# Kernel tuning notes

Measured on AMD Instinct MI355X. Metric: run time of the kernel, lower is better.

Reference implementation:

```python
import jax, jax.numpy as jnp
import numpy as np

B, T, I, H, C = 8192, 28, 28, 128, 10


def setup_inputs() -> dict:
    key = jax.random.key(0)
    ks = jax.random.split(key, 7)
    s_ih = 1.0 / np.sqrt(H)
    return {
        "x": jax.random.normal(ks[0], (B, T, I), dtype=jnp.float32),
        "W_ih": jax.random.normal(ks[1], (4 * H, I), dtype=jnp.float32) * s_ih,
        "W_hh": jax.random.normal(ks[2], (4 * H, H), dtype=jnp.float32) * s_ih,
        "b_ih": jax.random.normal(ks[3], (4 * H,), dtype=jnp.float32) * s_ih,
        "b_hh": jax.random.normal(ks[4], (4 * H,), dtype=jnp.float32) * s_ih,
        "W_fc": jax.random.normal(ks[5], (C, H), dtype=jnp.float32) * s_ih,
        "b_fc": jnp.zeros((C,), dtype=jnp.float32),
    }


def reference(x, W_ih, W_hh, b_ih, b_hh, W_fc, b_fc):
    # x: [B, T, I]. PyTorch LSTM gate order: i, f, g, o.
    b = b_ih + b_hh  # [4H]
    # Precompute input projections for all timesteps: [T, B, 4H]
    x_proj = jnp.einsum("bti,gi->tbg", x, W_ih) + b
    h0 = jnp.zeros((x.shape[0], H), dtype=x.dtype)
    c0 = jnp.zeros_like(h0)

    def step(carry, xp_t):
        h, c = carry
        gates = xp_t + h @ W_hh.T  # [B, 4H]
        i_g, f_g, g_g, o_g = jnp.split(gates, 4, axis=-1)
        i_g = jax.nn.sigmoid(i_g)
        f_g = jax.nn.sigmoid(f_g)
        g_g = jnp.tanh(g_g)
        o_g = jax.nn.sigmoid(o_g)
        c = f_g * c + i_g * g_g
        h = o_g * jnp.tanh(c)
        return (h, c), None

    (h_last, _), _ = jax.lax.scan(step, (h0, c0), x_proj)
    # outputs[:, -1, :] == final hidden state; fc + relu
    return jax.nn.relu(h_last @ W_fc.T + b_fc)
```

## Files before the change

### kernel.cpp

```cpp
#include <hip/hip_runtime.h>
#include <math.h>

typedef __attribute__((ext_vector_type(8))) _Float16 half8;
typedef __attribute__((ext_vector_type(4))) _Float16 half4;
typedef __attribute__((ext_vector_type(4))) float    f32x4;

#define TSTEPS 28
#define IDIM   28
#define HDIM   128
#define NKC    5
#define TILE_B 16
#define CDIM   10

#if __has_builtin(__builtin_amdgcn_exp2f)
#define EXP2F(x) __builtin_amdgcn_exp2f(x)
#else
#define EXP2F(x) exp2f(x)
#endif
#if __has_builtin(__builtin_amdgcn_rcpf)
#define RCPF(x) __builtin_amdgcn_rcpf(x)
#else
#define RCPF(x) (1.0f / (x))
#endif

#define NLOG2E (-1.44269504f)
#define P2LOG2E (2.88539008f)

__global__ __launch_bounds__(256) void pack_w(const float* __restrict__ Wih,
                                              const float* __restrict__ Whh,
                                              const float* __restrict__ bih,
                                              const float* __restrict__ bhh,
                                              _Float16* __restrict__ P) {
    int e = blockIdx.x * 256 + threadIdx.x;
    if (e >= NKC * 4 * 8 * 64 * 8) return;
    int j  = e & 7;
    int ln = (e >> 3) & 63;
    int w  = (e >> 9) & 7;
    int t  = (e >> 12) & 3;
    int kc = e >> 14;
    int k  = kc * 32 + ((ln >> 4) << 3) + j;
    int u  = w * 16 + (ln & 15);
    int g  = t * HDIM + u;
    float v = 0.f;
    if (k < HDIM)                   v = Whh[g * HDIM + k];
    else if (k < HDIM + IDIM)       v = Wih[g * IDIM + (k - HDIM)];
    else if (k == HDIM + IDIM)      v = bih[g] + bhh[g];
    float sc = (t == 2) ? P2LOG2E : NLOG2E;
    P[e] = (_Float16)(v * sc);
}

__global__ __launch_bounds__(512, 2) void lstm_kernel(
    const float* __restrict__ x,
    const _Float16* __restrict__ P,
    const float* __restrict__ Wfc,
    const float* __restrict__ b_fc,
    float* __restrict__ out)
{
    __shared__ __align__(16) _Float16 frag[2][NKC][64][8];
    __shared__ __align__(16) _Float16 Plds[4][8][64][8];
    __shared__ __align__(16) float hplain[TILE_B][HDIM + 4];

    const int tid = threadIdx.x;
    const int l   = tid & 63;
    const int w   = tid >> 6;
    const int b0  = blockIdx.x * TILE_B;

    {
        const float4* P4 = (const float4*)P;
        float4* dst = (float4*)Plds;
        #pragma unroll
        for (int q = 0; q < 4; ++q)
            dst[tid + q * 512] = P4[8192 + tid + q * 512];
    }
    half8 breg[4][4];
    {
        const half8* Pp = (const half8*)P;
        #pragma unroll
        for (int kc = 0; kc < 4; ++kc)
            #pragma unroll
            for (int t4 = 0; t4 < 4; ++t4)
                breg[t4][kc] = Pp[((kc * 4 + t4) * 8 + w) * 64 + l];
    }

    if (tid < 256) {
        float4 z = {0.f, 0.f, 0.f, 0.f};
        ((float4*)&frag[0][0][0][0])[tid] = z;
    }
    if (tid < 32) {
        int b = tid >> 4, i = tid & 15;
        half4 onev = {(_Float16)1.f, (_Float16)0.f, (_Float16)0.f, (_Float16)0.f};
        *(half4*)&frag[b][4][48 + i][4] = onev;
    }
    const int xrow = tid / 7, xg = tid % 7;
    if (tid < 112) {
        float4 xv = ((const float4*)(x + ((size_t)(b0 + xrow) * TSTEPS + 0) * IDIM))[xg];
        half4 hv = {(_Float16)xv.x, (_Float16)xv.y, (_Float16)xv.z, (_Float16)xv.w};
        *(half4*)&frag[0][4][xrow + 16 * (xg >> 1)][(xg & 1) * 4] = hv;
    }

    float cst[4] = {0.f, 0.f, 0.f, 0.f};
    const int u    = w * 16 + (l & 15);
    const int kc_h = w >> 1;
    const int quad = (2 * w + ((l >> 3) & 1)) & 3;
    const int jh   = l & 7;

    __syncthreads();

#if __has_builtin(__builtin_amdgcn_s_sleep)
    if (blockIdx.x & 256) __builtin_amdgcn_s_sleep(25);
#endif

    auto step = [&](int t, const _Float16 (*cur)[64][8], _Float16 (*nxt)[64][8]) {
        const bool last = (t == TSTEPS - 1);
        float4 xv;
        const bool doload = (t + 1 < TSTEPS) && (tid < 112);
        if (doload)
            xv = ((const float4*)(x + ((size_t)(b0 + xrow) * TSTEPS + (t + 1)) * IDIM))[xg];

        half8 a[NKC];
        #pragma unroll
        for (int kc = 0; kc < NKC; ++kc)
            a[kc] = *(const half8*)&cur[kc][l][0];

        f32x4 acc[4];
        #pragma unroll
        for (int t4 = 0; t4 < 4; ++t4) {
            f32x4 z = {0.f, 0.f, 0.f, 0.f};
            acc[t4] = z;
            #pragma unroll
            for (int kc = 0; kc < 4; ++kc)
                acc[t4] = __builtin_amdgcn_mfma_f32_16x16x32_f16(a[kc], breg[t4][kc], acc[t4], 0, 0, 0);
            half8 b = *(const half8*)&Plds[t4][w][l][0];
            acc[t4] = __builtin_amdgcn_mfma_f32_16x16x32_f16(a[4], b, acc[t4], 0, 0, 0);
        }

        #pragma unroll
        for (int r = 0; r < 4; ++r) {
            float Ei = EXP2F(acc[0][r]);
            float Ef = EXP2F(acc[1][r]);
            float Eg = EXP2F(acc[2][r]);
            float Eo = EXP2F(acc[3][r]);
            float Di = 1.f + Ei, Df = 1.f + Ef, Dg = 1.f + Eg, Do = 1.f + Eo;
            float Rif = RCPF(Di * Df);
            float Rgo = RCPF(Dg * Do);
            float is = Rif * Df, fs = Rif * Di;
            float gt = 1.f - 2.f * (Rgo * Do);
            float os = Rgo * Dg;
            float c  = fs * cst[r] + is * gt;
            cst[r] = c;
            float tc = 1.f - 2.f * RCPF(1.f + EXP2F(c * P2LOG2E));
            float h  = os * tc;
            int m = ((l >> 4) << 2) + r;
            nxt[kc_h][m + 16 * quad][jh] = (_Float16)h;
            if (last) hplain[m][u] = h;
        }
        if (doload) {
            half4 hv = {(_Float16)xv.x, (_Float16)xv.y, (_Float16)xv.z, (_Float16)xv.w};
            *(half4*)&nxt[4][xrow + 16 * (xg >> 1)][(xg & 1) * 4] = hv;
        }
        __syncthreads();
    };

    for (int tt = 0; tt < TSTEPS; tt += 2) {
        step(tt,     frag[0], frag[1]);
        step(tt + 1, frag[1], frag[0]);
    }

    if (tid < TILE_B * CDIM) {
        int row = tid / CDIM, c = tid % CDIM;
        const float4* hv = (const float4*)&hplain[row][0];
        const float4* wf = (const float4*)(Wfc + c * HDIM);
        float s = b_fc[c];
        #pragma unroll
        for (int q = 0; q < 32; ++q) {
            float4 a4 = hv[q], b4 = wf[q];
            s += a4.x * b4.x + a4.y * b4.y + a4.z * b4.z + a4.w * b4.w;
        }
        out[(size_t)(b0 + row) * CDIM + c] = fmaxf(s, 0.f);
    }
}

extern "C" void kernel_launch(void* const* d_in, const int* in_sizes, int n_in,
                              void* d_out, int out_size, void* d_ws, size_t ws_size,
                              hipStream_t stream) {
    const float* x   = (const float*)d_in[0];
    const float* Wih = (const float*)d_in[1];
    const float* Whh = (const float*)d_in[2];
    const float* bih = (const float*)d_in[3];
    const float* bhh = (const float*)d_in[4];
    const float* Wfc = (const float*)d_in[5];
    const float* bfc = (const float*)d_in[6];
    float* out = (float*)d_out;
    _Float16* P = (_Float16*)d_ws;

    hipLaunchKernelGGL(pack_w, dim3(320), dim3(256), 0, stream, Wih, Whh, bih, bhh, P);
    hipLaunchKernelGGL(lstm_kernel, dim3(8192 / TILE_B), dim3(512), 0, stream,
                       x, P, Wfc, bfc, out);
}
```

Before: 125.7 us.

## Pipeline next-step input-projection MFMA ahead of recurrent dependency and spread x loads

Moves the x/bias chunk (kc=4) MFMA for step t+1 so it issues right after the gate nonlinearities of step t, before the h write and barrier. The recurrent critical path then only carries the four W_hh MFMA chunks. x is now prefetched two steps ahead into the current buffer, and the loader threads are spread across all 8 waves (14 lanes each) instead of the first 112 threads. The accumulator becomes loop-carried, which raises register pressure, and the correctness of the buffer reuse now depends on careful ordering.

```diff
diff --git a/kernel.cpp b/kernel.cpp
--- a/kernel.cpp
+++ b/kernel.cpp
@@ -91,11 +91,21 @@
         half4 onev = {(_Float16)1.f, (_Float16)0.f, (_Float16)0.f, (_Float16)0.f};
         *(half4*)&frag[b][4][48 + i][4] = onev;
     }
-    const int xrow = tid / 7, xg = tid % 7;
-    if (tid < 112) {
-        float4 xv = ((const float4*)(x + ((size_t)(b0 + xrow) * TSTEPS + 0) * IDIM))[xg];
-        half4 hv = {(_Float16)xv.x, (_Float16)xv.y, (_Float16)xv.z, (_Float16)xv.w};
-        *(half4*)&frag[0][4][xrow + 16 * (xg >> 1)][(xg & 1) * 4] = hv;
+
+    const bool isldr = (l < 14);
+    const int  lj    = w * 14 + l;
+    const int  xr    = lj / 7, xg = lj % 7;
+    const int  xslot = xr + 16 * (xg >> 1);
+    const int  xoff  = (xg & 1) * 4;
+
+    if (isldr) {
+        const float4* xs = (const float4*)(x + (size_t)(b0 + xr) * (TSTEPS * IDIM));
+        float4 x0 = xs[xg];
+        float4 x1 = xs[7 + xg];
+        half4 h0 = {(_Float16)x0.x, (_Float16)x0.y, (_Float16)x0.z, (_Float16)x0.w};
+        half4 h1 = {(_Float16)x1.x, (_Float16)x1.y, (_Float16)x1.z, (_Float16)x1.w};
+        *(half4*)&frag[0][4][xslot][xoff] = h0;
+        *(half4*)&frag[1][4][xslot][xoff] = h1;
     }
 
     float cst[4] = {0.f, 0.f, 0.f, 0.f};
@@ -110,30 +120,45 @@
     if (blockIdx.x & 256) __builtin_amdgcn_s_sleep(25);
 #endif
 
-    auto step = [&](int t, const _Float16 (*cur)[64][8], _Float16 (*nxt)[64][8]) {
+    f32x4 acc[4];
+
+    auto kc4_mfma = [&](const _Float16 (*buf)[64][8]) {
+        half8 a4 = *(const half8*)&buf[4][l][0];
+        #pragma unroll
+        for (int t4 = 0; t4 < 4; ++t4) {
+            half8 b = *(const half8*)&Plds[t4][w][l][0];
+            acc[t4] = __builtin_amdgcn_mfma_f32_16x16x32_f16(a4, b, acc[t4], 0, 0, 0);
+        }
+    };
+    auto zero_acc = [&]() {
+        #pragma unroll
+        for (int t4 = 0; t4 < 4; ++t4) { f32x4 z = {0.f, 0.f, 0.f, 0.f}; acc[t4] = z; }
+    };
+
+    zero_acc();
+    kc4_mfma(frag[0]);
+
+    for (int t = 0; t < TSTEPS; ++t) {
+        const _Float16 (*cur)[64][8] = frag[t & 1];
+        _Float16 (*nxt)[64][8] = frag[(t & 1) ^ 1];
         const bool last = (t == TSTEPS - 1);
+
         float4 xv;
-        const bool doload = (t + 1 < TSTEPS) && (tid < 112);
+        const bool doload = (t + 2 < TSTEPS) && isldr;
         if (doload)
-            xv = ((const float4*)(x + ((size_t)(b0 + xrow) * TSTEPS + (t + 1)) * IDIM))[xg];
-
-        half8 a[NKC];
-        #pragma unroll
-        for (int kc = 0; kc < NKC; ++kc)
+            xv = ((const float4*)(x + (size_t)(b0 + xr) * (TSTEPS * IDIM)))[(t + 2) * 7 + xg];
+
+        half8 a[4];
+        #pragma unroll
+        for (int kc = 0; kc < 4; ++kc)
             a[kc] = *(const half8*)&cur[kc][l][0];
-
-        f32x4 acc[4];
-        #pragma unroll
-        for (int t4 = 0; t4 < 4; ++t4) {
-            f32x4 z = {0.f, 0.f, 0.f, 0.f};
-            acc[t4] = z;
+        #pragma unroll
+        for (int t4 = 0; t4 < 4; ++t4)
             #pragma unroll
             for (int kc = 0; kc < 4; ++kc)
                 acc[t4] = __builtin_amdgcn_mfma_f32_16x16x32_f16(a[kc], breg[t4][kc], acc[t4], 0, 0, 0);
-            half8 b = *(const half8*)&Plds[t4][w][l][0];
-            acc[t4] = __builtin_amdgcn_mfma_f32_16x16x32_f16(a[4], b, acc[t4], 0, 0, 0);
-        }
-
+
+        float hv[4];
         #pragma unroll
         for (int r = 0; r < 4; ++r) {
             float Ei = EXP2F(acc[0][r]);
@@ -149,31 +174,35 @@
             float c  = fs * cst[r] + is * gt;
             cst[r] = c;
             float tc = 1.f - 2.f * RCPF(1.f + EXP2F(c * P2LOG2E));
-            float h  = os * tc;
+            hv[r] = os * tc;
+        }
+
+        if (!last) {
+            zero_acc();
+            kc4_mfma(nxt);
+        }
+
+        #pragma unroll
+        for (int r = 0; r < 4; ++r) {
             int m = ((l >> 4) << 2) + r;
-            nxt[kc_h][m + 16 * quad][jh] = (_Float16)h;
-            if (last) hplain[m][u] = h;
+            nxt[kc_h][m + 16 * quad][jh] = (_Float16)hv[r];
+            if (last) hplain[m][u] = hv[r];
         }
         if (doload) {
-            half4 hv = {(_Float16)xv.x, (_Float16)xv.y, (_Float16)xv.z, (_Float16)xv.w};
-            *(half4*)&nxt[4][xrow + 16 * (xg >> 1)][(xg & 1) * 4] = hv;
+            half4 hc = {(_Float16)xv.x, (_Float16)xv.y, (_Float16)xv.z, (_Float16)xv.w};
+            *(half4*)&((_Float16 (*)[64][8])cur)[4][xslot][xoff] = hc;
         }
         __syncthreads();
-    };
-
-    for (int tt = 0; tt < TSTEPS; tt += 2) {
-        step(tt,     frag[0], frag[1]);
-        step(tt + 1, frag[1], frag[0]);
     }
 
     if (tid < TILE_B * CDIM) {
         int row = tid / CDIM, c = tid % CDIM;
-        const float4* hv = (const float4*)&hplain[row][0];
-        const float4* wf = (const float4*)(Wfc + c * HDIM);
+        const float4* hv4 = (const float4*)&hplain[row][0];
+        const float4* wf  = (const float4*)(Wfc + c * HDIM);
         float s = b_fc[c];
         #pragma unroll
         for (int q = 0; q < 32; ++q) {
-            float4 a4 = hv[q], b4 = wf[q];
+            float4 a4 = hv4[q], b4 = wf[q];
             s += a4.x * b4.x + a4.y * b4.y + a4.z * b4.z + a4.w * b4.w;
         }
         out[(size_t)(b0 + row) * CDIM + c] = fmaxf(s, 0.f);
```

After: 132.3 us. 1.05x slower.
